# Kernel tuning notes

Hardware: AMD Instinct MI355X
Metric: run time of the kernel (lower is better)

Reference implementation:

```python
import jax, jax.numpy as jnp
import numpy as np

def setup_inputs() -> dict:
    key = jax.random.key(0)
    k1, k2, k3, k4, k5 = jax.random.split(key, 5)
    H = 1024
    B, T = 32, 1024
    hidden = jax.random.normal(k1, (1, B, H), dtype=jnp.float32)
    encoder_outputs = jax.random.normal(k2, (B, T, H), dtype=jnp.float32)
    # nn.Linear(2H, H): weight [H, 2H], bias [H]
    bound = 1.0 / np.sqrt(2 * H)
    W = jax.random.uniform(k3, (H, 2 * H), minval=-bound, maxval=bound, dtype=jnp.float32)
    b = jax.random.uniform(k4, (H,), minval=-bound, maxval=bound, dtype=jnp.float32)
    v = jax.random.uniform(k5, (H,), dtype=jnp.float32)  # torch.rand
    return {"hidden": hidden, "encoder_outputs": encoder_outputs, "W": W, "b": b, "v": v}

def reference(hidden, encoder_outputs, W, b, v):
    B = hidden.shape[1]
    H = hidden.shape[2]
    h = jnp.transpose(hidden, (1, 0, 2)).reshape(B, -1)  # [B, H]
    # Split Linear(2H->H): cat([h_rep, enc]) @ W.T == h @ Wh.T + enc @ We.T
    Wh, We = W[:, :H], W[:, H:]
    # [B,1,H] + [B,T,H] -> [B,T,H]
    pre = jnp.tanh((h @ Wh.T + b)[:, None, :] + jnp.einsum('bth,gh->btg', encoder_outputs, We))
    energies = jnp.einsum('bth,h->bt', pre, v)  # [B, T]
    return jax.nn.softmax(energies, axis=1)[:, None, :]  # [B, 1, T]
```

## Files before the change

kernel.cpp:

```cpp
#include <hip/hip_runtime.h>
#include <hip/hip_fp16.h>

typedef _Float16 half8   __attribute__((ext_vector_type(8)));
typedef _Float16 half4_t __attribute__((ext_vector_type(4)));
typedef float    f32x4   __attribute__((ext_vector_type(4)));

#define HDIM  1024
#define BATCH 32
#define TLEN  1024
#define M_TOT (BATCH * TLEN)

#define BM 128
#define BN 128
#define BKF 32
#define LDA 40

__global__ void prep_k(const float* __restrict__ W, const float* __restrict__ hidden,
                       const float* __restrict__ bias, _Float16* __restrict__ We16,
                       float* __restrict__ q, float* __restrict__ energ) {
    const int bid = blockIdx.x;
    const int t = threadIdx.x;
    if (bid < 1024) {
        int idx = bid * 256 + t;
        int g  = idx >> 8;
        int k4 = idx & 255;
        float4 f = *reinterpret_cast<const float4*>(W + (size_t)g * 2048 + 1024 + k4 * 4);
        half4_t h;
        h[0] = (_Float16)f.x; h[1] = (_Float16)f.y; h[2] = (_Float16)f.z; h[3] = (_Float16)f.w;
        *reinterpret_cast<half4_t*>(We16 + (size_t)idx * 4) = h;
    } else if (bid < 2048) {
        int g = bid - 1024;
        int wave = t >> 6, lane = t & 63;
        float acc[BATCH];
#pragma unroll
        for (int b = 0; b < BATCH; b++) acc[b] = 0.f;
        const float* wr = W + (size_t)g * 2048;
        for (int h = t; h < HDIM; h += 256) {
            float w = wr[h];
#pragma unroll
            for (int b = 0; b < BATCH; b++) acc[b] = fmaf(w, hidden[b * HDIM + h], acc[b]);
        }
        __shared__ float sm[4 * BATCH];
#pragma unroll
        for (int b = 0; b < BATCH; b++) {
            float s = acc[b];
#pragma unroll
            for (int off = 32; off >= 1; off >>= 1) s += __shfl_xor(s, off);
            if (lane == 0) sm[wave * BATCH + b] = s;
        }
        __syncthreads();
        if (t < BATCH) {
            float s = sm[t] + sm[BATCH + t] + sm[2 * BATCH + t] + sm[3 * BATCH + t];
            q[t * HDIM + g] = s + bias[g];
        }
    } else {
        energ[(bid - 2048) * 256 + t] = 0.f;
    }
}

__global__ void enc_convert_k(const float* __restrict__ enc, _Float16* __restrict__ enc16) {
    size_t i = ((size_t)blockIdx.x * blockDim.x + threadIdx.x) * 8;
    float4 f0 = *reinterpret_cast<const float4*>(enc + i);
    float4 f1 = *reinterpret_cast<const float4*>(enc + i + 4);
    half8 h;
    h[0] = (_Float16)f0.x; h[1] = (_Float16)f0.y; h[2] = (_Float16)f0.z; h[3] = (_Float16)f0.w;
    h[4] = (_Float16)f1.x; h[5] = (_Float16)f1.y; h[6] = (_Float16)f1.z; h[7] = (_Float16)f1.w;
    *reinterpret_cast<half8*>(enc16 + i) = h;
}

__device__ __forceinline__ void async16(const void* g, void* l) {
    __builtin_amdgcn_global_load_lds(
        (const __attribute__((address_space(1))) void*)g,
        (__attribute__((address_space(3))) void*)l, 16, 0, 0);
}

__global__ __launch_bounds__(256, 4)
void attn_gemm_lds_k(const _Float16* __restrict__ enc16,
                     const _Float16* __restrict__ We16,
                     const float* __restrict__ q, const float* __restrict__ v,
                     float* __restrict__ energies) {
    __shared__ _Float16 As[2][BM * BKF];
    __shared__ _Float16 Bs[2][BN * BKF];

    const int tid  = threadIdx.x;
    const int id   = blockIdx.x;
    const int xcd  = id & 7;
    const int w    = id >> 3;
    const int m0   = (xcd * 32 + (w >> 3)) * BM;
    const int n0   = (w & 7) * BN;
    const int wave = tid >> 6;
    const int lane = tid & 63;
    const int quad = lane >> 4;
    const int l16  = lane & 15;
    const int wm   = (wave & 1) * 64;
    const int wn   = (wave >> 1) * 64;

    f32x4 acc[4][4];
#pragma unroll
    for (int i = 0; i < 4; i++)
#pragma unroll
        for (int j = 0; j < 4; j++) acc[i][j] = {0.f, 0.f, 0.f, 0.f};

    const int srow   = wave * 32 + (lane >> 2);
    const int fchunk = (lane & 3) ^ ((lane >> 3) & 3);
    const _Float16* gA = enc16 + (size_t)(m0 + srow) * HDIM + fchunk * 8;
    const _Float16* gB = We16  + (size_t)(n0 + srow) * HDIM + fchunk * 8;
    const size_t istep = (size_t)16 * HDIM;
    const int ldst = wave * 1024;

    async16(gA, &As[0][ldst]);
    async16(gA + istep, &As[0][ldst + 512]);
    async16(gB, &Bs[0][ldst]);
    async16(gB + istep, &Bs[0][ldst + 512]);
    __syncthreads();

    int aoff[4], boff[4];
#pragma unroll
    for (int i = 0; i < 4; i++) {
        int ra = wm + i * 16 + l16;
        int rb = wn + i * 16 + l16;
        aoff[i] = ra * BKF + ((quad ^ ((ra >> 1) & 3)) * 8);
        boff[i] = rb * BKF + ((quad ^ ((rb >> 1) & 3)) * 8);
    }

    for (int it = 0; it < HDIM / BKF; it++) {
        const int p = it & 1;
        if (it + 1 < HDIM / BKF) {
            const int kn = (it + 1) * BKF;
            async16(gA + kn, &As[1 - p][ldst]);
            async16(gA + kn + istep, &As[1 - p][ldst + 512]);
            async16(gB + kn, &Bs[1 - p][ldst]);
            async16(gB + kn + istep, &Bs[1 - p][ldst + 512]);
        }

        half8 af[4], bf[4];
#pragma unroll
        for (int i = 0; i < 4; i++) {
            af[i] = *reinterpret_cast<const half8*>(&As[p][aoff[i]]);
            bf[i] = *reinterpret_cast<const half8*>(&Bs[p][boff[i]]);
        }
#pragma unroll
        for (int mi = 0; mi < 4; mi++)
#pragma unroll
            for (int ni = 0; ni < 4; ni++)
                acc[mi][ni] = __builtin_amdgcn_mfma_f32_16x16x32_f16(af[mi], bf[ni], acc[mi][ni], 0, 0, 0);

        __syncthreads();
    }

    const int bidx = m0 >> 10;
    float qv[4], vv[4];
#pragma unroll
    for (int ni = 0; ni < 4; ni++) {
        int g = n0 + wn + ni * 16 + l16;
        qv[ni] = q[bidx * HDIM + g];
        vv[ni] = v[g];
    }
#pragma unroll
    for (int mi = 0; mi < 4; mi++) {
#pragma unroll
        for (int r = 0; r < 4; r++) {
            int row = wm + mi * 16 + quad * 4 + r;
            float s = 0.f;
#pragma unroll
            for (int ni = 0; ni < 4; ni++) {
                float pre = acc[mi][ni][r] + qv[ni];
                float e = __expf(2.f * pre);
                float th = 1.f - 2.f / (e + 1.f);
                s = fmaf(th, vv[ni], s);
            }
            s += __shfl_xor(s, 1);
            s += __shfl_xor(s, 2);
            s += __shfl_xor(s, 4);
            s += __shfl_xor(s, 8);
            if (l16 == 0) atomicAdd(&energies[m0 + row], s);
        }
    }
}

__global__ __launch_bounds__(256, 2)
void attn_gemm_k(const float* __restrict__ enc, const _Float16* __restrict__ We16,
                 const float* __restrict__ q, const float* __restrict__ v,
                 float* __restrict__ energies) {
    __shared__ _Float16 As[BM * LDA];
    __shared__ _Float16 Bs[BN * LDA];

    const int tid  = threadIdx.x;
    const int m0   = blockIdx.x * BM;
    const int n0   = blockIdx.y * BN;
    const int wave = tid >> 6;
    const int lane = tid & 63;
    const int quad = lane >> 4;
    const int l16  = lane & 15;
    const int wm   = (wave & 1) * 64;
    const int wn   = (wave >> 1) * 64;

    const int srow = tid >> 1;
    const int scol = (tid & 1) * 16;

    f32x4 acc[4][4];
#pragma unroll
    for (int i = 0; i < 4; i++)
#pragma unroll
        for (int j = 0; j < 4; j++) acc[i][j] = {0.f, 0.f, 0.f, 0.f};

    const float*    ag = enc  + (size_t)(m0 + srow) * HDIM + scol;
    const _Float16* bg = We16 + (size_t)(n0 + srow) * HDIM + scol;
    _Float16* aw = &As[srow * LDA + scol];
    _Float16* bw = &Bs[srow * LDA + scol];

    for (int k0 = 0; k0 < HDIM; k0 += 32) {
        float4 a0 = *reinterpret_cast<const float4*>(ag + k0 + 0);
        float4 a1 = *reinterpret_cast<const float4*>(ag + k0 + 4);
        float4 a2 = *reinterpret_cast<const float4*>(ag + k0 + 8);
        float4 a3 = *reinterpret_cast<const float4*>(ag + k0 + 12);
        float4 b0 = *reinterpret_cast<const float4*>(bg + k0);
        float4 b1 = *reinterpret_cast<const float4*>(bg + k0 + 8);

        __syncthreads();

        half8 ha0, ha1;
        ha0[0] = (_Float16)a0.x; ha0[1] = (_Float16)a0.y; ha0[2] = (_Float16)a0.z; ha0[3] = (_Float16)a0.w;
        ha0[4] = (_Float16)a1.x; ha0[5] = (_Float16)a1.y; ha0[6] = (_Float16)a1.z; ha0[7] = (_Float16)a1.w;
        ha1[0] = (_Float16)a2.x; ha1[1] = (_Float16)a2.y; ha1[2] = (_Float16)a2.z; ha1[3] = (_Float16)a2.w;
        ha1[4] = (_Float16)a3.x; ha1[5] = (_Float16)a3.y; ha1[6] = (_Float16)a3.z; ha1[7] = (_Float16)a3.w;
        *reinterpret_cast<half8*>(aw)     = ha0;
        *reinterpret_cast<half8*>(aw + 8) = ha1;
        *reinterpret_cast<float4*>(bw)     = b0;
        *reinterpret_cast<float4*>(bw + 8) = b1;

        __syncthreads();

        half8 af[4], bf[4];
#pragma unroll
        for (int i = 0; i < 4; i++) {
            af[i] = *reinterpret_cast<const half8*>(&As[(wm + i * 16 + l16) * LDA + quad * 8]);
            bf[i] = *reinterpret_cast<const half8*>(&Bs[(wn + i * 16 + l16) * LDA + quad * 8]);
        }
#pragma unroll
        for (int mi = 0; mi < 4; mi++)
#pragma unroll
            for (int ni = 0; ni < 4; ni++)
                acc[mi][ni] = __builtin_amdgcn_mfma_f32_16x16x32_f16(af[mi], bf[ni], acc[mi][ni], 0, 0, 0);
    }

    const int bidx = m0 >> 10;
    float qv[4], vv[4];
#pragma unroll
    for (int ni = 0; ni < 4; ni++) {
        int g = n0 + wn + ni * 16 + l16;
        qv[ni] = q[bidx * HDIM + g];
        vv[ni] = v[g];
    }
#pragma unroll
    for (int mi = 0; mi < 4; mi++) {
#pragma unroll
        for (int r = 0; r < 4; r++) {
            int row = wm + mi * 16 + quad * 4 + r;
            float s = 0.f;
#pragma unroll
            for (int ni = 0; ni < 4; ni++) {
                float pre = acc[mi][ni][r] + qv[ni];
                float e = __expf(2.f * pre);
                float th = 1.f - 2.f / (e + 1.f);
                s = fmaf(th, vv[ni], s);
            }
            s += __shfl_xor(s, 1);
            s += __shfl_xor(s, 2);
            s += __shfl_xor(s, 4);
            s += __shfl_xor(s, 8);
            if (l16 == 0) atomicAdd(&energies[m0 + row], s);
        }
    }
}

__global__ void softmax_k(const float* __restrict__ energies, float* __restrict__ out) {
    int b = blockIdx.x;
    int t = threadIdx.x;
    int wave = t >> 6, lane = t & 63;
    __shared__ float smax[4], ssum[4];
    float e[4];
#pragma unroll
    for (int i = 0; i < 4; i++) e[i] = energies[b * TLEN + t + i * 256];
    float m = fmaxf(fmaxf(e[0], e[1]), fmaxf(e[2], e[3]));
#pragma unroll
    for (int off = 32; off >= 1; off >>= 1) m = fmaxf(m, __shfl_xor(m, off));
    if (lane == 0) smax[wave] = m;
    __syncthreads();
    float M = fmaxf(fmaxf(smax[0], smax[1]), fmaxf(smax[2], smax[3]));
    float x[4]; float s = 0.f;
#pragma unroll
    for (int i = 0; i < 4; i++) { x[i] = __expf(e[i] - M); s += x[i]; }
#pragma unroll
    for (int off = 32; off >= 1; off >>= 1) s += __shfl_xor(s, off);
    if (lane == 0) ssum[wave] = s;
    __syncthreads();
    float S = ssum[0] + ssum[1] + ssum[2] + ssum[3];
    float inv = 1.f / S;
#pragma unroll
    for (int i = 0; i < 4; i++) out[b * TLEN + t + i * 256] = x[i] * inv;
}

extern "C" void kernel_launch(void* const* d_in, const int* in_sizes, int n_in,
                              void* d_out, int out_size, void* d_ws, size_t ws_size,
                              hipStream_t stream) {
    const float* hidden = (const float*)d_in[0];
    const float* enc    = (const float*)d_in[1];
    const float* W      = (const float*)d_in[2];
    const float* bias   = (const float*)d_in[3];
    const float* v      = (const float*)d_in[4];
    float* out = (float*)d_out;

    char* ws = (char*)d_ws;
    float*    q     = (float*)ws;
    float*    energ = (float*)(ws + 131072);
    _Float16* We16  = (_Float16*)(ws + 262144);
    _Float16* enc16 = (_Float16*)(ws + 262144 + 2097152);
    const size_t need_fast = 262144 + 2097152 + (size_t)M_TOT * HDIM * 2;

    prep_k<<<dim3(2176), 256, 0, stream>>>(W, hidden, bias, We16, q, energ);
    if (ws_size >= need_fast) {
        enc_convert_k<<<dim3((size_t)M_TOT * HDIM / 8 / 256), 256, 0, stream>>>(enc, enc16);
        attn_gemm_lds_k<<<dim3(2048), 256, 0, stream>>>(enc16, We16, q, v, energ);
    } else {
        attn_gemm_k<<<dim3(256, 8), 256, 0, stream>>>(enc, We16, q, v, energ);
    }
    softmax_k<<<dim3(BATCH), 256, 0, stream>>>(energ, out);
}
```

Measured before the change: 327.0 us.

## Enlarge GEMM tile to 256x128 and stage loads through registers

The fp16 MFMA GEMM now uses a 256x128 block tile, with each wave computing 128x64 and holding 8x4 accumulators. This raises arithmetic intensity and halves the block count. The async global-to-LDS loads are replaced by register-staged prefetch: global loads are issued before the MFMAs and written into the other LDS buffer afterward. The cost is higher register pressure, with occupancy bounds dropped from 4 to 2 blocks per CU, and LDS writes added to the critical path.

```diff
diff --git a/kernel.cpp b/kernel.cpp
--- a/kernel.cpp
+++ b/kernel.cpp
@@ -10,9 +10,10 @@
 #define TLEN  1024
 #define M_TOT (BATCH * TLEN)
 
-#define BM 128
-#define BN 128
+#define BMF 256
+#define BNF 128
 #define BKF 32
+#define NIT (HDIM / BKF)
 #define LDA 40
 
 __global__ void prep_k(const float* __restrict__ W, const float* __restrict__ hidden,
@@ -68,83 +69,96 @@
     *reinterpret_cast<half8*>(enc16 + i) = h;
 }
 
-__device__ __forceinline__ void async16(const void* g, void* l) {
-    __builtin_amdgcn_global_load_lds(
-        (const __attribute__((address_space(1))) void*)g,
-        (__attribute__((address_space(3))) void*)l, 16, 0, 0);
-}
-
-__global__ __launch_bounds__(256, 4)
-void attn_gemm_lds_k(const _Float16* __restrict__ enc16,
+__global__ __launch_bounds__(256, 2)
+void attn_gemm_big_k(const _Float16* __restrict__ enc16,
                      const _Float16* __restrict__ We16,
                      const float* __restrict__ q, const float* __restrict__ v,
                      float* __restrict__ energies) {
-    __shared__ _Float16 As[2][BM * BKF];
-    __shared__ _Float16 Bs[2][BN * BKF];
+    __shared__ _Float16 As[2][BMF * BKF];
+    __shared__ _Float16 Bs[2][BNF * BKF];
 
     const int tid  = threadIdx.x;
     const int id   = blockIdx.x;
     const int xcd  = id & 7;
     const int w    = id >> 3;
-    const int m0   = (xcd * 32 + (w >> 3)) * BM;
-    const int n0   = (w & 7) * BN;
+    const int m0   = (xcd * 16 + (w >> 3)) * BMF;
+    const int n0   = (w & 7) * BNF;
     const int wave = tid >> 6;
     const int lane = tid & 63;
     const int quad = lane >> 4;
     const int l16  = lane & 15;
-    const int wm   = (wave & 1) * 64;
+    const int wm   = (wave & 1) * 128;
     const int wn   = (wave >> 1) * 64;
 
-    f32x4 acc[4][4];
-#pragma unroll
-    for (int i = 0; i < 4; i++)
+    f32x4 acc[8][4];
+#pragma unroll
+    for (int i = 0; i < 8; i++)
 #pragma unroll
         for (int j = 0; j < 4; j++) acc[i][j] = {0.f, 0.f, 0.f, 0.f};
 
-    const int srow   = wave * 32 + (lane >> 2);
-    const int fchunk = (lane & 3) ^ ((lane >> 3) & 3);
-    const _Float16* gA = enc16 + (size_t)(m0 + srow) * HDIM + fchunk * 8;
-    const _Float16* gB = We16  + (size_t)(n0 + srow) * HDIM + fchunk * 8;
-    const size_t istep = (size_t)16 * HDIM;
-    const int ldst = wave * 1024;
-
-    async16(gA, &As[0][ldst]);
-    async16(gA + istep, &As[0][ldst + 512]);
-    async16(gB, &Bs[0][ldst]);
-    async16(gB + istep, &Bs[0][ldst + 512]);
+    const _Float16* gA = enc16 + (size_t)(m0 + tid) * HDIM;
+    const int brow = tid >> 1;
+    const int bch  = (tid & 1) * 2;
+    const _Float16* gB = We16 + (size_t)(n0 + brow) * HDIM + bch * 8;
+    const int aswz = (tid >> 1) & 3;
+    const int bswz = (brow >> 1) & 3;
+    const int abase = tid * BKF;
+    const int bbase = brow * BKF;
+
+    half8 rA[4], rB[2];
+
+#pragma unroll
+    for (int j = 0; j < 4; j++) rA[j] = *reinterpret_cast<const half8*>(gA + j * 8);
+    rB[0] = *reinterpret_cast<const half8*>(gB);
+    rB[1] = *reinterpret_cast<const half8*>(gB + 8);
+#pragma unroll
+    for (int j = 0; j < 4; j++)
+        *reinterpret_cast<half8*>(&As[0][abase + ((j ^ aswz) * 8)]) = rA[j];
+    *reinterpret_cast<half8*>(&Bs[0][bbase + (((bch + 0) ^ bswz) * 8)]) = rB[0];
+    *reinterpret_cast<half8*>(&Bs[0][bbase + (((bch + 1) ^ bswz) * 8)]) = rB[1];
     __syncthreads();
 
-    int aoff[4], boff[4];
+    int aoff[8], boff[4];
+#pragma unroll
+    for (int i = 0; i < 8; i++) {
+        int ra = wm + i * 16 + l16;
+        aoff[i] = ra * BKF + ((quad ^ ((ra >> 1) & 3)) * 8);
+    }
 #pragma unroll
     for (int i = 0; i < 4; i++) {
-        int ra = wm + i * 16 + l16;
         int rb = wn + i * 16 + l16;
-        aoff[i] = ra * BKF + ((quad ^ ((ra >> 1) & 3)) * 8);
         boff[i] = rb * BKF + ((quad ^ ((rb >> 1) & 3)) * 8);
     }
 
-    for (int it = 0; it < HDIM / BKF; it++) {
+    for (int it = 0; it < NIT; it++) {
         const int p = it & 1;
-        if (it + 1 < HDIM / BKF) {
-            const int kn = (it + 1) * BKF;
-            async16(gA + kn, &As[1 - p][ldst]);
-            async16(gA + kn + istep, &As[1 - p][ldst + 512]);
-            async16(gB + kn, &Bs[1 - p][ldst]);
-            async16(gB + kn + istep, &Bs[1 - p][ldst + 512]);
-        }
-
-        half8 af[4], bf[4];
-#pragma unroll
-        for (int i = 0; i < 4; i++) {
-            af[i] = *reinterpret_cast<const half8*>(&As[p][aoff[i]]);
-            bf[i] = *reinterpret_cast<const half8*>(&Bs[p][boff[i]]);
-        }
-#pragma unroll
-        for (int mi = 0; mi < 4; mi++)
+        if (it + 1 < NIT) {
+            const int k = (it + 1) * BKF;
+#pragma unroll
+            for (int j = 0; j < 4; j++) rA[j] = *reinterpret_cast<const half8*>(gA + k + j * 8);
+            rB[0] = *reinterpret_cast<const half8*>(gB + k);
+            rB[1] = *reinterpret_cast<const half8*>(gB + k + 8);
+        }
+
+        half8 af[8], bf[4];
+#pragma unroll
+        for (int i = 0; i < 8; i++) af[i] = *reinterpret_cast<const half8*>(&As[p][aoff[i]]);
+#pragma unroll
+        for (int i = 0; i < 4; i++) bf[i] = *reinterpret_cast<const half8*>(&Bs[p][boff[i]]);
+
+#pragma unroll
+        for (int mi = 0; mi < 8; mi++)
 #pragma unroll
             for (int ni = 0; ni < 4; ni++)
                 acc[mi][ni] = __builtin_amdgcn_mfma_f32_16x16x32_f16(af[mi], bf[ni], acc[mi][ni], 0, 0, 0);
 
+        if (it + 1 < NIT) {
+#pragma unroll
+            for (int j = 0; j < 4; j++)
+                *reinterpret_cast<half8*>(&As[1 - p][abase + ((j ^ aswz) * 8)]) = rA[j];
+            *reinterpret_cast<half8*>(&Bs[1 - p][bbase + (((bch + 0) ^ bswz) * 8)]) = rB[0];
+            *reinterpret_cast<half8*>(&Bs[1 - p][bbase + (((bch + 1) ^ bswz) * 8)]) = rB[1];
+        }
         __syncthreads();
     }
 
@@ -157,7 +171,7 @@
         vv[ni] = v[g];
     }
 #pragma unroll
-    for (int mi = 0; mi < 4; mi++) {
+    for (int mi = 0; mi < 8; mi++) {
 #pragma unroll
         for (int r = 0; r < 4; r++) {
             int row = wm + mi * 16 + quad * 4 + r;
@@ -182,12 +196,12 @@
 void attn_gemm_k(const float* __restrict__ enc, const _Float16* __restrict__ We16,
                  const float* __restrict__ q, const float* __restrict__ v,
                  float* __restrict__ energies) {
-    __shared__ _Float16 As[BM * LDA];
-    __shared__ _Float16 Bs[BN * LDA];
+    __shared__ _Float16 As[128 * LDA];
+    __shared__ _Float16 Bs[128 * LDA];
 
     const int tid  = threadIdx.x;
-    const int m0   = blockIdx.x * BM;
-    const int n0   = blockIdx.y * BN;
+    const int m0   = blockIdx.x * 128;
+    const int n0   = blockIdx.y * 128;
     const int wave = tid >> 6;
     const int lane = tid & 63;
     const int quad = lane >> 4;
@@ -321,7 +335,7 @@
     prep_k<<<dim3(2176), 256, 0, stream>>>(W, hidden, bias, We16, q, energ);
     if (ws_size >= need_fast) {
         enc_convert_k<<<dim3((size_t)M_TOT * HDIM / 8 / 256), 256, 0, stream>>>(enc, enc16);
-        attn_gemm_lds_k<<<dim3(2048), 256, 0, stream>>>(enc16, We16, q, v, energ);
+        attn_gemm_big_k<<<dim3(1024), 256, 0, stream>>>(enc16, We16, q, v, energ);
     } else {
         attn_gemm_k<<<dim3(256, 8), 256, 0, stream>>>(enc, We16, q, v, energ);
     }
```

New measurement: 373.0 us. 14.1% more time.
